# Kernel optimization log

Measured on AMD Instinct MI355X. Metric: run time of the kernel, lower is better.

Reference implementation:

```python
import jax, jax.numpy as jnp
import numpy as np

N_USER = 200000
N_ITEM = 100000
E = 1000000
H = 128
IN_USER = 64
IN_ITEM = 128
OUT = 16
L = 2  # n_layers
NEG_SLOPE = 0.01  # F.leaky_relu default


def _leaky(x):
    return jnp.where(x >= 0, x, NEG_SLOPE * x)


def _sage(x_src, x_dst, src, dst, n_dst, Wl, bl, Wr):
    """PyG SAGEConv (aggr='mean'): lin_l(mean_{j->i} x_j) + lin_r(x_i)."""
    agg = jax.ops.segment_sum(x_src[src], dst, num_segments=n_dst)  # [n_dst, H]
    cnt = jax.ops.segment_sum(jnp.ones((src.shape[0],), x_src.dtype), dst, num_segments=n_dst)
    mean = agg / jnp.maximum(cnt, 1.0)[:, None]
    return mean @ Wl + bl + x_dst @ Wr


def setup_inputs() -> dict:
    key = jax.random.key(0)
    ks = jax.random.split(key, 32)
    s = 0.05
    inp = {
        "x_user": jax.random.normal(ks[0], (N_USER, IN_USER), jnp.float32),
        "x_item": jax.random.normal(ks[1], (N_ITEM, IN_ITEM), jnp.float32),
        "src_rates": jax.random.randint(ks[2], (E,), 0, N_USER, jnp.int32),
        "dst_rates": jax.random.randint(ks[3], (E,), 0, N_ITEM, jnp.int32),
        "src_rated": jax.random.randint(ks[4], (E,), 0, N_ITEM, jnp.int32),
        "dst_rated": jax.random.randint(ks[5], (E,), 0, N_USER, jnp.int32),
        "src_fol": jax.random.randint(ks[6], (E,), 0, N_USER, jnp.int32),
        "dst_fol": jax.random.randint(ks[7], (E,), 0, N_USER, jnp.int32),
        # input projections (per node type)
        "W_in_user": s * jax.random.normal(ks[8], (IN_USER, H), jnp.float32),
        "b_in_user": jnp.zeros((H,), jnp.float32),
        "W_in_item": s * jax.random.normal(ks[9], (IN_ITEM, H), jnp.float32),
        "b_in_item": jnp.zeros((H,), jnp.float32),
        # per-layer SAGEConv params, stacked over layers [L, ...]
        "Wl_rates": s * jax.random.normal(ks[10], (L, H, H), jnp.float32),
        "bl_rates": jnp.zeros((L, H), jnp.float32),
        "Wr_rates": s * jax.random.normal(ks[11], (L, H, H), jnp.float32),
        "Wl_rated": s * jax.random.normal(ks[12], (L, H, H), jnp.float32),
        "bl_rated": jnp.zeros((L, H), jnp.float32),
        "Wr_rated": s * jax.random.normal(ks[13], (L, H, H), jnp.float32),
        "Wl_fol": s * jax.random.normal(ks[14], (L, H, H), jnp.float32),
        "bl_fol": jnp.zeros((L, H), jnp.float32),
        "Wr_fol": s * jax.random.normal(ks[15], (L, H, H), jnp.float32),
        # output head
        "W_out": s * jax.random.normal(ks[16], (H, OUT), jnp.float32),
        "b_out": jnp.zeros((OUT,), jnp.float32),
    }
    return inp


def reference(x_user, x_item, src_rates, dst_rates, src_rated, dst_rated,
              src_fol, dst_fol, W_in_user, b_in_user, W_in_item, b_in_item,
              Wl_rates, bl_rates, Wr_rates, Wl_rated, bl_rated, Wr_rated,
              Wl_fol, bl_fol, Wr_fol, W_out, b_out):
    hu = x_user @ W_in_user + b_in_user  # [N_USER, H]
    hi = x_item @ W_in_item + b_in_item  # [N_ITEM, H]
    for l in range(L):
        # user->item ('rates')
        hi_new = _sage(hu, hi, src_rates, dst_rates, N_ITEM,
                       Wl_rates[l], bl_rates[l], Wr_rates[l])
        # item->user ('rated_by') + user->user ('follows'), HeteroConv aggr='sum'
        hu_new = (_sage(hi, hu, src_rated, dst_rated, N_USER,
                        Wl_rated[l], bl_rated[l], Wr_rated[l])
                  + _sage(hu, hu, src_fol, dst_fol, N_USER,
                          Wl_fol[l], bl_fol[l], Wr_fol[l]))
        hu, hi = hu_new, hi_new
        if l != L - 1:
            hu = _leaky(hu)
            hi = _leaky(hi)
    return hu @ W_out + b_out  # target_node == 'user'
```

## Files before the change

### kernel.cpp

```cpp
#include <hip/hip_runtime.h>
#include <cstdint>

typedef short short8 __attribute__((ext_vector_type(8)));
typedef float floatx4 __attribute__((ext_vector_type(4)));

constexpr int NU = 200000;
constexpr int NI = 100000;
constexpr int NEDGE = 1000000;
constexpr int HD = 128;
constexpr int HH = HD * HD;
constexpr int BUK = 1024;
constexpr int EPB = 4096;
constexpr int EPT = 16;
constexpr int MAXBUK = 256;
constexpr int NBLK = (NEDGE + EPB - 1) / EPB;
constexpr int NB_I = (NI + BUK - 1) / BUK;
constexpr int NB_U = (NU + BUK - 1) / BUK;
constexpr int LROW = 136;

__device__ __forceinline__ float bits2f(short s) {
    return __uint_as_float(((unsigned int)(unsigned short)s) << 16);
}
__device__ __forceinline__ short f2bits(float f) {
    unsigned int u = __float_as_uint(f);
    unsigned int lsb = (u >> 16) & 1u;
    u += 0x7fffu + lsb;
    return (short)(u >> 16);
}

__global__ __launch_bounds__(256) void k_cnt3(const int* __restrict__ dst0,
                                              const int* __restrict__ dst1,
                                              const int* __restrict__ dst2,
                                              int* __restrict__ cnts) {
    __shared__ int cnt[MAXBUK];
    const int g = blockIdx.x / NBLK;
    const int blk = blockIdx.x % NBLK;
    const int* dst = (g == 0) ? dst0 : (g == 1) ? dst1 : dst2;
    int t = threadIdx.x;
    for (int b = t; b < MAXBUK; b += 256) cnt[b] = 0;
    __syncthreads();
    const int e0 = blk * EPB + t * EPT;
#pragma unroll
    for (int i = 0; i < EPT; ++i) {
        int e = e0 + i;
        if (e < NEDGE) atomicAdd(&cnt[dst[e] >> 10], 1);
    }
    __syncthreads();
    for (int b = t; b < MAXBUK; b += 256)
        cnts[(size_t)(g * NBLK + blk) * MAXBUK + b] = cnt[b];
}

__global__ __launch_bounds__(256) void k_bases3(const int* __restrict__ cnts,
                                                int* __restrict__ base,
                                                int* __restrict__ bbase,
                                                int* __restrict__ off0,
                                                int* __restrict__ off1,
                                                int* __restrict__ off2) {
    __shared__ int s[256];
    const int g = blockIdx.x;
    const int t = threadIdx.x;
    int tot = 0;
    for (int blk = 0; blk < NBLK; ++blk)
        tot += cnts[(size_t)(g * NBLK + blk) * MAXBUK + t];
    s[t] = tot;
    __syncthreads();
    for (int d = 1; d < 256; d <<= 1) {
        int u = (t >= d) ? s[t - d] : 0;
        __syncthreads();
        s[t] += u;
        __syncthreads();
    }
    int bb = s[t] - tot;
    bbase[g * 257 + t] = bb;
    if (t == 255) bbase[g * 257 + 256] = bb + tot;
    int run = bb;
    for (int blk = 0; blk < NBLK; ++blk) {
        size_t idx = (size_t)(g * NBLK + blk) * MAXBUK + t;
        base[idx] = run;
        run += cnts[idx];
    }
    if (t == 0) {
        if (g == 0) off0[NI] = NEDGE;
        else if (g == 1) off1[NU] = NEDGE;
        else off2[NU] = NEDGE;
    }
}

__global__ __launch_bounds__(256) void k_part3(const int* __restrict__ src0,
                                               const int* __restrict__ dst0,
                                               const int* __restrict__ src1,
                                               const int* __restrict__ dst1,
                                               const int* __restrict__ src2,
                                               const int* __restrict__ dst2,
                                               const int* __restrict__ base,
                                               int* __restrict__ pairs) {
    __shared__ int cnt[MAXBUK];
    __shared__ int bas[MAXBUK];
    const int g = blockIdx.x / NBLK;
    const int blk = blockIdx.x % NBLK;
    const int* src = (g == 0) ? src0 : (g == 1) ? src1 : src2;
    const int* dst = (g == 0) ? dst0 : (g == 1) ? dst1 : dst2;
    int* pg = pairs + (size_t)g * NEDGE;
    int t = threadIdx.x;
    for (int b = t; b < MAXBUK; b += 256) cnt[b] = 0;
    __syncthreads();
    const int e0 = blk * EPB + t * EPT;
    int sv[EPT], dv[EPT], rk[EPT];
#pragma unroll
    for (int i = 0; i < EPT; ++i) {
        int e = e0 + i;
        bool ok = e < NEDGE;
        dv[i] = ok ? dst[e] : 0;
        sv[i] = ok ? src[e] : 0;
    }
#pragma unroll
    for (int i = 0; i < EPT; ++i)
        rk[i] = (e0 + i < NEDGE) ? atomicAdd(&cnt[dv[i] >> 10], 1) : 0;
    __syncthreads();
    for (int b = t; b < MAXBUK; b += 256)
        bas[b] = base[(size_t)(g * NBLK + blk) * MAXBUK + b];
    __syncthreads();
#pragma unroll
    for (int i = 0; i < EPT; ++i) {
        if (e0 + i < NEDGE)
            pg[bas[dv[i] >> 10] + rk[i]] = sv[i] | ((dv[i] & 1023) << 18);
    }
}

__global__ __launch_bounds__(256) void k_place3(const int* __restrict__ pairs,
                                                const int* __restrict__ bbase,
                                                int* __restrict__ off0, int* __restrict__ esrc0,
                                                int* __restrict__ off1, int* __restrict__ esrc1,
                                                int* __restrict__ off2, int* __restrict__ esrc2) {
    __shared__ int cnt[BUK];
    __shared__ int ts[256];
    int bi = blockIdx.x;
    int g, bloc, N;
    int* off;
    int* esrc;
    if (bi < NB_I) { g = 0; bloc = bi; N = NI; off = off0; esrc = esrc0; }
    else if (bi < NB_I + NB_U) { g = 1; bloc = bi - NB_I; N = NU; off = off1; esrc = esrc1; }
    else { g = 2; bloc = bi - NB_I - NB_U; N = NU; off = off2; esrc = esrc2; }
    const int* pg = pairs + (size_t)g * NEDGE;
    const int b0 = bbase[g * 257 + bloc];
    const int b1 = bbase[g * 257 + bloc + 1];
    const int t = threadIdx.x;
    for (int i = t; i < BUK; i += 256) cnt[i] = 0;
    __syncthreads();
    for (int j = b0 + t; j < b1; j += 256) atomicAdd(&cnt[pg[j] >> 18], 1);
    __syncthreads();
    const int idx = t * 4;
    int c0 = cnt[idx], c1 = cnt[idx + 1], c2 = cnt[idx + 2], c3 = cnt[idx + 3];
    int ssum = c0 + c1 + c2 + c3;
    ts[t] = ssum;
    __syncthreads();
    for (int d = 1; d < 256; d <<= 1) {
        int u = (t >= d) ? ts[t - d] : 0;
        __syncthreads();
        ts[t] += u;
        __syncthreads();
    }
    int o = b0 + ts[t] - ssum;
    const int n0 = bloc * BUK;
    int cc[4] = {c0, c1, c2, c3};
#pragma unroll
    for (int i = 0; i < 4; ++i) {
        int n = n0 + idx + i;
        if (n < N) off[n] = o;
        cnt[idx + i] = o;
        o += cc[i];
    }
    __syncthreads();
    for (int j = b0 + t; j < b1; j += 256) {
        int p = pg[j];
        int pos = atomicAdd(&cnt[p >> 18], 1);
        esrc[pos] = p & 0x3FFFF;
    }
}

__global__ void k_pack(short* __restrict__ dst, const float* __restrict__ A,
                       const float* __restrict__ B, const float* __restrict__ B2,
                       int KA, int KBr, int NCOL) {
    int l = threadIdx.x;
    int kbt = (KA + KBr) >> 5;
    int nt = blockIdx.x / kbt;
    int kb = blockIdx.x % kbt;
    int col = nt * 16 + (l & 15);
    int k0 = kb * 32 + (l >> 4) * 8;
    short8 o;
#pragma unroll
    for (int j = 0; j < 8; ++j) {
        int k = k0 + j;
        float f;
        if (k < KA) {
            f = A[(size_t)k * NCOL + col];
        } else {
            int k2 = k - KA;
            f = B[(size_t)k2 * NCOL + col];
            if (B2) f += B2[(size_t)k2 * NCOL + col];
        }
        o[j] = f2bits(f);
    }
    *(short8*)(dst + ((size_t)blockIdx.x * 64 + l) * 8) = o;
}

__global__ void k_pack3(short* __restrict__ dst, const float* __restrict__ A,
                        const float* __restrict__ B, const float* __restrict__ C1,
                        const float* __restrict__ C2) {
    int l = threadIdx.x;
    constexpr int kbt = 12;
    int nt = blockIdx.x / kbt;
    int kb = blockIdx.x % kbt;
    int col = nt * 16 + (l & 15);
    int k0 = kb * 32 + (l >> 4) * 8;
    short8 o;
#pragma unroll
    for (int j = 0; j < 8; ++j) {
        int k = k0 + j;
        float f;
        if (k < 128) f = A[(size_t)k * 128 + col];
        else if (k < 256) f = B[(size_t)(k - 128) * 128 + col];
        else f = C1[(size_t)(k - 256) * 128 + col] + C2[(size_t)(k - 256) * 128 + col];
        o[j] = f2bits(f);
    }
    *(short8*)(dst + ((size_t)blockIdx.x * 64 + l) * 8) = o;
}

__global__ void k_foldW(float* __restrict__ dst, const float* __restrict__ Wa,
                        const float* __restrict__ Wb, const float* __restrict__ Wo,
                        int colOff, int NC) {
    int k = blockIdx.x;
    int c = threadIdx.x;
    float a = 0.f;
    for (int t = 0; t < 128; ++t) {
        float w = Wa[(size_t)k * 128 + t];
        if (Wb) w += Wb[(size_t)k * 128 + t];
        a += w * Wo[t * 16 + c];
    }
    dst[(size_t)k * NC + colOff + c] = a;
}

__global__ void k_bfold(float* __restrict__ dst, const float* __restrict__ bl1,
                        const float* __restrict__ bl2, const float* __restrict__ Wo,
                        const float* __restrict__ bo) {
    int c = threadIdx.x;
    float a = 0.f;
    for (int t = 0; t < 128; ++t) a += (bl1[t] + bl2[t]) * Wo[t * 16 + c];
    dst[c] = a + bo[c];
}

__global__ void k_addbias(float* __restrict__ dst, const float* __restrict__ a,
                          const float* __restrict__ b) {
    int i = threadIdx.x;
    dst[i] = a[i] + b[i];
}

__device__ __forceinline__ void gather_mean(const short* __restrict__ Xsrc,
                                            const int* __restrict__ off,
                                            const int* __restrict__ esrc,
                                            int ar, int ksub, float macc[4][8]) {
#pragma unroll
    for (int kb = 0; kb < 4; ++kb)
#pragma unroll
        for (int i = 0; i < 8; ++i) macc[kb][i] = 0.f;

    const int s = off[ar], e = off[ar + 1];
    int j = s;
    for (; j + 4 <= e; j += 4) {
        const int i0 = esrc[j], i1 = esrc[j + 1], i2 = esrc[j + 2], i3 = esrc[j + 3];
        const short* p0 = Xsrc + (size_t)i0 * HD + ksub;
        const short* p1 = Xsrc + (size_t)i1 * HD + ksub;
        const short* p2 = Xsrc + (size_t)i2 * HD + ksub;
        const short* p3 = Xsrc + (size_t)i3 * HD + ksub;
        short8 v0[4], v1[4], v2[4], v3[4];
#pragma unroll
        for (int kb = 0; kb < 4; ++kb) {
            v0[kb] = *(const short8*)(p0 + kb * 32);
            v1[kb] = *(const short8*)(p1 + kb * 32);
            v2[kb] = *(const short8*)(p2 + kb * 32);
            v3[kb] = *(const short8*)(p3 + kb * 32);
        }
#pragma unroll
        for (int kb = 0; kb < 4; ++kb)
#pragma unroll
            for (int i = 0; i < 8; ++i)
                macc[kb][i] += (bits2f(v0[kb][i]) + bits2f(v1[kb][i]))
                             + (bits2f(v2[kb][i]) + bits2f(v3[kb][i]));
    }
    for (; j < e; ++j) {
        const short* xp = Xsrc + (size_t)esrc[j] * HD + ksub;
#pragma unroll
        for (int kb = 0; kb < 4; ++kb) {
            short8 v = *(const short8*)(xp + kb * 32);
#pragma unroll
            for (int i = 0; i < 8; ++i) macc[kb][i] += bits2f(v[i]);
        }
    }
    const int d = e - s;
    const float inv = 1.f / (float)(d > 0 ? d : 1);
#pragma unroll
    for (int kb = 0; kb < 4; ++kb)
#pragma unroll
        for (int i = 0; i < 8; ++i) macc[kb][i] *= inv;
}

template <int NT2>
__device__ __forceinline__ void fold_epi(const floatx4* acc8, const float* __restrict__ bias,
                                         const short* __restrict__ pFold,
                                         short* __restrict__ Y, int r0, int lane,
                                         short* my, int M) {
    const int colL = lane & 15;
    const int g = lane >> 4;
#pragma unroll
    for (int nt = 0; nt < 8; ++nt) {
        float bv = bias[nt * 16 + colL];
#pragma unroll
        for (int r = 0; r < 4; ++r) {
            float x = acc8[nt][r] + bv;
            x = (x >= 0.f) ? x : 0.01f * x;
            my[(g * 4 + r) * LROW + nt * 16 + colL] = f2bits(x);
        }
    }
    short8 af[4];
    const short* rp = my + colL * LROW + g * 8;
#pragma unroll
    for (int kb = 0; kb < 4; ++kb) af[kb] = *(const short8*)(rp + kb * 32);

    floatx4 a2[NT2];
#pragma unroll
    for (int nt2 = 0; nt2 < NT2; ++nt2) a2[nt2] = (floatx4){0.f, 0.f, 0.f, 0.f};
    const short8* wp = (const short8*)pFold + lane;
#pragma unroll
    for (int nt2 = 0; nt2 < NT2; ++nt2)
#pragma unroll
        for (int kb = 0; kb < 4; ++kb) {
            short8 b = wp[(nt2 * 4 + kb) * 64];
            a2[nt2] = __builtin_amdgcn_mfma_f32_16x16x32_bf16(af[kb], b, a2[nt2], 0, 0, 0);
        }

    const int rbase = r0 + g * 4;
#pragma unroll
    for (int nt2 = 0; nt2 < NT2; ++nt2)
#pragma unroll
        for (int r = 0; r < 4; ++r) {
            int row = rbase + r;
            if (row < M) Y[(size_t)row * (NT2 * 16) + nt2 * 16 + colL] = f2bits(a2[nt2][r]);
        }
}

__global__ __launch_bounds__(256) void k_sage_all(
        const short* __restrict__ hu, const short* __restrict__ hi,
        const int* __restrict__ off_rates, const int* __restrict__ esrc_rates,
        const int* __restrict__ off_rated, const int* __restrict__ esrc_rated,
        const int* __restrict__ off_fol, const int* __restrict__ esrc_fol,
        const short* __restrict__ WpI, const float* __restrict__ biasI,
        const short* __restrict__ pYI,
        const short* __restrict__ WpU, const float* __restrict__ biasU,
        const short* __restrict__ pYU,
        short* __restrict__ YI, short* __restrict__ YZ, int gU) {
    __shared__ short stage[4 * 16 * LROW];
    const int lane = threadIdx.x & 63;
    const int wv = threadIdx.x >> 6;
    short* my = stage + wv * (16 * LROW);
    const int ksub = (lane >> 4) * 8;

    if ((int)blockIdx.x < gU) {
        const int r0 = blockIdx.x * 64 + wv * 16;
        int ar = r0 + (lane & 15);
        if (ar >= NU) ar = NU - 1;

        short8 afrag[12];
        {
            float macc[4][8];
            gather_mean(hi, off_rated, esrc_rated, ar, ksub, macc);
#pragma unroll
            for (int kb = 0; kb < 4; ++kb) {
                short8 f;
#pragma unroll
                for (int i = 0; i < 8; ++i) f[i] = f2bits(macc[kb][i]);
                afrag[kb] = f;
            }
            gather_mean(hu, off_fol, esrc_fol, ar, ksub, macc);
#pragma unroll
            for (int kb = 0; kb < 4; ++kb) {
                short8 f;
#pragma unroll
                for (int i = 0; i < 8; ++i) f[i] = f2bits(macc[kb][i]);
                afrag[4 + kb] = f;
            }
        }
        {
            const short* p = hu + (size_t)ar * HD + ksub;
#pragma unroll
            for (int kb = 0; kb < 4; ++kb) afrag[8 + kb] = *(const short8*)(p + kb * 32);
        }

        floatx4 acc[8];
#pragma unroll
        for (int nt = 0; nt < 8; ++nt) acc[nt] = (floatx4){0.f, 0.f, 0.f, 0.f};
        const short8* wp = (const short8*)WpU + lane;
#pragma unroll
        for (int nt = 0; nt < 8; ++nt)
#pragma unroll
            for (int kb = 0; kb < 12; ++kb) {
                short8 b = wp[(nt * 12 + kb) * 64];
                acc[nt] = __builtin_amdgcn_mfma_f32_16x16x32_bf16(afrag[kb], b, acc[nt], 0, 0, 0);
            }

        fold_epi<2>(acc, biasU, pYU, YZ, r0, lane, my, NU);
    } else {
        const int b = blockIdx.x - gU;
        const int r0 = b * 64 + wv * 16;
        int ar = r0 + (lane & 15);
        if (ar >= NI) ar = NI - 1;

        short8 afrag[8];
        {
            float macc[4][8];
            gather_mean(hu, off_rates, esrc_rates, ar, ksub, macc);
#pragma unroll
            for (int kb = 0; kb < 4; ++kb) {
                short8 f;
#pragma unroll
                for (int i = 0; i < 8; ++i) f[i] = f2bits(macc[kb][i]);
                afrag[kb] = f;
            }
            const short* p = hi + (size_t)ar * HD + ksub;
#pragma unroll
            for (int kb = 0; kb < 4; ++kb) afrag[4 + kb] = *(const short8*)(p + kb * 32);
        }

        floatx4 acc[8];
#pragma unroll
        for (int nt = 0; nt < 8; ++nt) acc[nt] = (floatx4){0.f, 0.f, 0.f, 0.f};
        const short8* wp = (const short8*)WpI + lane;
#pragma unroll
        for (int nt = 0; nt < 8; ++nt)
#pragma unroll
            for (int kb = 0; kb < 8; ++kb) {
                short8 b = wp[(nt * 8 + kb) * 64];
                acc[nt] = __builtin_amdgcn_mfma_f32_16x16x32_bf16(afrag[kb], b, acc[nt], 0, 0, 0);
            }

        fold_epi<1>(acc, biasI, pYI, YI, r0, lane, my, NI);
    }
}

template <int KB1>
__device__ __forceinline__ void mm_body(int bid, const float* __restrict__ A1,
                                        const short* __restrict__ Wp,
                                        const float* __restrict__ bias,
                                        short* __restrict__ C, int M,
                                        int lane, int wv) {
    const int r0 = bid * 128 + wv * 32;
    const int ksub = (lane >> 4) * 8;
    short8 afrag[2][KB1];
#pragma unroll
    for (int h = 0; h < 2; ++h) {
        int ar = r0 + h * 16 + (lane & 15);
        if (ar >= M) ar = M - 1;
        const float* p = A1 + (size_t)ar * (KB1 * 32) + ksub;
#pragma unroll
        for (int kb = 0; kb < KB1; ++kb) {
            short8 f;
#pragma unroll
            for (int j = 0; j < 8; ++j) f[j] = f2bits(p[kb * 32 + j]);
            afrag[h][kb] = f;
        }
    }
    floatx4 acc[2][8];
#pragma unroll
    for (int h = 0; h < 2; ++h)
#pragma unroll
        for (int nt = 0; nt < 8; ++nt) acc[h][nt] = (floatx4){0.f, 0.f, 0.f, 0.f};
    const short8* wp = (const short8*)Wp + lane;
#pragma unroll
    for (int nt = 0; nt < 8; ++nt)
#pragma unroll
        for (int kb = 0; kb < KB1; ++kb) {
            short8 b = wp[(nt * KB1 + kb) * 64];
            acc[0][nt] = __builtin_amdgcn_mfma_f32_16x16x32_bf16(afrag[0][kb], b, acc[0][nt], 0, 0, 0);
            acc[1][nt] = __builtin_amdgcn_mfma_f32_16x16x32_bf16(afrag[1][kb], b, acc[1][nt], 0, 0, 0);
        }
    const int col = lane & 15;
#pragma unroll
    for (int h = 0; h < 2; ++h) {
        const int rbase = r0 + h * 16 + (lane >> 4) * 4;
#pragma unroll
        for (int nt = 0; nt < 8; ++nt) {
            float bv = bias[nt * 16 + col];
#pragma unroll
            for (int r = 0; r < 4; ++r) {
                int row = rbase + r;
                if (row < M)
                    C[(size_t)row * 128 + nt * 16 + col] = f2bits(acc[h][nt][r] + bv);
            }
        }
    }
}

__global__ __launch_bounds__(256) void k_mm2(const float* __restrict__ xu,
                                             const short* __restrict__ pWu,
                                             const float* __restrict__ bu,
                                             short* __restrict__ hu,
                                             const float* __restrict__ xi,
                                             const short* __restrict__ pWi,
                                             const float* __restrict__ bi,
                                             short* __restrict__ hi, int gU2) {
    const int lane = threadIdx.x & 63;
    const int wv = threadIdx.x >> 6;
    if ((int)blockIdx.x < gU2)
        mm_body<2>(blockIdx.x, xu, pWu, bu, hu, NU, lane, wv);
    else
        mm_body<4>(blockIdx.x - gU2, xi, pWi, bi, hi, NI, lane, wv);
}

__global__ __launch_bounds__(256) void k_out(const short* __restrict__ YZ,
                                             const short* __restrict__ YI,
                                             const int* __restrict__ off_f,
                                             const int* __restrict__ esrc_f,
                                             const int* __restrict__ off_r,
                                             const int* __restrict__ esrc_r,
                                             const float* __restrict__ bias16,
                                             float* __restrict__ out, int N) {
    int t = threadIdx.x;
    int node = blockIdx.x * 128 + (t >> 1);
    int half = t & 1;
    if (node >= N) return;
    const int c0 = half * 8;

    float a[8] = {0.f, 0.f, 0.f, 0.f, 0.f, 0.f, 0.f, 0.f};
    {
        const int s = off_f[node], e = off_f[node + 1];
        int j = s;
        for (; j + 4 <= e; j += 4) {
            short8 v0 = *(const short8*)(YZ + (size_t)esrc_f[j] * 32 + c0);
            short8 v1 = *(const short8*)(YZ + (size_t)esrc_f[j + 1] * 32 + c0);
            short8 v2 = *(const short8*)(YZ + (size_t)esrc_f[j + 2] * 32 + c0);
            short8 v3 = *(const short8*)(YZ + (size_t)esrc_f[j + 3] * 32 + c0);
#pragma unroll
            for (int i = 0; i < 8; ++i)
                a[i] += (bits2f(v0[i]) + bits2f(v1[i])) + (bits2f(v2[i]) + bits2f(v3[i]));
        }
        for (; j < e; ++j) {
            short8 v = *(const short8*)(YZ + (size_t)esrc_f[j] * 32 + c0);
#pragma unroll
            for (int i = 0; i < 8; ++i) a[i] += bits2f(v[i]);
        }
        int d = e - s;
        float inv = 1.f / (float)(d > 0 ? d : 1);
#pragma unroll
        for (int i = 0; i < 8; ++i) a[i] *= inv;
    }
    {
        float b[8] = {0.f, 0.f, 0.f, 0.f, 0.f, 0.f, 0.f, 0.f};
        const int s = off_r[node], e = off_r[node + 1];
        int j = s;
        for (; j + 4 <= e; j += 4) {
            short8 v0 = *(const short8*)(YI + (size_t)esrc_r[j] * 16 + c0);
            short8 v1 = *(const short8*)(YI + (size_t)esrc_r[j + 1] * 16 + c0);
            short8 v2 = *(const short8*)(YI + (size_t)esrc_r[j + 2] * 16 + c0);
            short8 v3 = *(const short8*)(YI + (size_t)esrc_r[j + 3] * 16 + c0);
#pragma unroll
            for (int i = 0; i < 8; ++i)
                b[i] += (bits2f(v0[i]) + bits2f(v1[i])) + (bits2f(v2[i]) + bits2f(v3[i]));
        }
        for (; j < e; ++j) {
            short8 v = *(const short8*)(YI + (size_t)esrc_r[j] * 16 + c0);
#pragma unroll
            for (int i = 0; i < 8; ++i) b[i] += bits2f(v[i]);
        }
        int d = e - s;
        float inv = 1.f / (float)(d > 0 ? d : 1);
#pragma unroll
        for (int i = 0; i < 8; ++i) a[i] += b[i] * inv;
    }
    short8 z = *(const short8*)(YZ + (size_t)node * 32 + 16 + c0);
#pragma unroll
    for (int i = 0; i < 8; ++i)
        out[(size_t)node * 16 + c0 + i] = a[i] + bits2f(z[i]) + bias16[c0 + i];
}

extern "C" void kernel_launch(void* const* d_in, const int* in_sizes, int n_in,
                              void* d_out, int out_size, void* d_ws, size_t ws_size,
                              hipStream_t stream) {
    const float* x_user    = (const float*)d_in[0];
    const float* x_item    = (const float*)d_in[1];
    const int* src_rates   = (const int*)d_in[2];
    const int* dst_rates   = (const int*)d_in[3];
    const int* src_rated   = (const int*)d_in[4];
    const int* dst_rated   = (const int*)d_in[5];
    const int* src_fol     = (const int*)d_in[6];
    const int* dst_fol     = (const int*)d_in[7];
    const float* W_in_user = (const float*)d_in[8];
    const float* b_in_user = (const float*)d_in[9];
    const float* W_in_item = (const float*)d_in[10];
    const float* b_in_item = (const float*)d_in[11];
    const float* Wl_rates  = (const float*)d_in[12];
    const float* bl_rates  = (const float*)d_in[13];
    const float* Wr_rates  = (const float*)d_in[14];
    const float* Wl_rated  = (const float*)d_in[15];
    const float* bl_rated  = (const float*)d_in[16];
    const float* Wr_rated  = (const float*)d_in[17];
    const float* Wl_fol    = (const float*)d_in[18];
    const float* bl_fol    = (const float*)d_in[19];
    const float* Wr_fol    = (const float*)d_in[20];
    const float* W_out     = (const float*)d_in[21];
    const float* b_out     = (const float*)d_in[22];
    float* out = (float*)d_out;

    char* w = (char*)d_ws;
    size_t used = 0;
    auto alloc = [&](size_t bytes) -> void* {
        void* p = w + used;
        used += (bytes + 255) & ~(size_t)255;
        return p;
    };
    short* hu_a = (short*)alloc((size_t)NU * HD * 2);
    short* hi_a = (short*)alloc((size_t)NI * HD * 2);
    short* YZ   = (short*)alloc((size_t)NU * 32 * 2);
    short* YI   = (short*)alloc((size_t)NI * 16 * 2);

    int* off_rates  = (int*)alloc((size_t)(NI + 1) * 4);
    int* esrc_rates = (int*)alloc((size_t)NEDGE * 4);
    int* off_rated  = (int*)alloc((size_t)(NU + 1) * 4);
    int* esrc_rated = (int*)alloc((size_t)NEDGE * 4);
    int* off_fol    = (int*)alloc((size_t)(NU + 1) * 4);
    int* esrc_fol   = (int*)alloc((size_t)NEDGE * 4);
    int* pairs      = (int*)alloc((size_t)3 * NEDGE * 4);
    int* cnts       = (int*)alloc((size_t)3 * NBLK * MAXBUK * 4);
    int* base       = (int*)alloc((size_t)3 * NBLK * MAXBUK * 4);
    int* bbase      = (int*)alloc((size_t)3 * 257 * 4);

    short* pWu    = (short*)alloc(8 * 2 * 64 * 8 * 2);
    short* pWi    = (short*)alloc(8 * 4 * 64 * 8 * 2);
    short* pRates0 = (short*)alloc(8 * 8 * 64 * 8 * 2);
    short* pUser0  = (short*)alloc(8 * 12 * 64 * 8 * 2);
    float* WfU    = (float*)alloc(128 * 32 * 4);
    float* WfI    = (float*)alloc(128 * 16 * 4);
    short* pYU    = (short*)alloc(2 * 4 * 64 * 8 * 2);
    short* pYI    = (short*)alloc(1 * 4 * 64 * 8 * 2);
    float* bSum0  = (float*)alloc(128 * 4);
    float* bias16 = (float*)alloc(16 * 4);
    if (used > ws_size) return;

    k_cnt3<<<3 * NBLK, 256, 0, stream>>>(dst_rates, dst_rated, dst_fol, cnts);
    k_bases3<<<3, 256, 0, stream>>>(cnts, base, bbase, off_rates, off_rated, off_fol);
    k_part3<<<3 * NBLK, 256, 0, stream>>>(src_rates, dst_rates, src_rated, dst_rated,
                                          src_fol, dst_fol, base, pairs);
    k_place3<<<NB_I + 2 * NB_U, 256, 0, stream>>>(pairs, bbase,
                                                  off_rates, esrc_rates,
                                                  off_rated, esrc_rated,
                                                  off_fol, esrc_fol);

    k_pack<<<16, 64, 0, stream>>>(pWu, W_in_user, nullptr, nullptr, 64, 0, 128);
    k_pack<<<32, 64, 0, stream>>>(pWi, W_in_item, nullptr, nullptr, 128, 0, 128);
    k_pack<<<64, 64, 0, stream>>>(pRates0, Wl_rates, Wr_rates, nullptr, 128, 128, 128);
    k_pack3<<<96, 64, 0, stream>>>(pUser0, Wl_rated, Wl_fol, Wr_rated, Wr_fol);
    k_addbias<<<1, 128, 0, stream>>>(bSum0, bl_rated, bl_fol);
    k_foldW<<<128, 16, 0, stream>>>(WfU, Wl_fol + HH,   nullptr,     W_out, 0, 32);
    k_foldW<<<128, 16, 0, stream>>>(WfU, Wr_rated + HH, Wr_fol + HH, W_out, 16, 32);
    k_foldW<<<128, 16, 0, stream>>>(WfI, Wl_rated + HH, nullptr,     W_out, 0, 16);
    k_pack<<<8, 64, 0, stream>>>(pYU, WfU, nullptr, nullptr, 128, 0, 32);
    k_pack<<<4, 64, 0, stream>>>(pYI, WfI, nullptr, nullptr, 128, 0, 16);
    k_bfold<<<1, 16, 0, stream>>>(bias16, bl_rated + 128, bl_fol + 128, W_out, b_out);

    const int gU2 = (NU + 127) / 128;
    const int gI2 = (NI + 127) / 128;
    const int gU  = (NU + 63) / 64;
    const int gI  = (NI + 63) / 64;

    k_mm2<<<gU2 + gI2, 256, 0, stream>>>(x_user, pWu, b_in_user, hu_a,
                                         x_item, pWi, b_in_item, hi_a, gU2);

    k_sage_all<<<gU + gI, 256, 0, stream>>>(
        hu_a, hi_a, off_rates, esrc_rates, off_rated, esrc_rated, off_fol, esrc_fol,
        pRates0, bl_rates, pYI, pUser0, bSum0, pYU, YI, YZ, gU);

    k_out<<<(NU + 127) / 128, 256, 0, stream>>>(
        YZ, YI, off_fol, esrc_fol, off_rated, esrc_rated, bias16, out, NU);
}
```

Baseline: 444.8 us.

## Quantize node embeddings to per-row int8 for neighbor gathers

The input projection kernel now also writes an 8-bit offset-quantized copy of each user and item embedding, with a per-row scale. The SAGE kernel gathers neighbors from this copy and dequantizes it with an FMA plus a final bias correction. The aim is to halve the gather memory traffic, which dominates the aggregation. In exchange it adds quantization error to the aggregated means, writes extra storage in the projection kernel, and removes the 4-way edge unrolling, which reduces memory-level parallelism.

```diff
diff --git a/kernel.cpp b/kernel.cpp
--- a/kernel.cpp
+++ b/kernel.cpp
@@ -3,6 +3,7 @@
 
 typedef short short8 __attribute__((ext_vector_type(8)));
 typedef float floatx4 __attribute__((ext_vector_type(4)));
+typedef unsigned char uchar;
 
 constexpr int NU = 200000;
 constexpr int NI = 100000;
@@ -255,53 +256,40 @@
     dst[i] = a[i] + b[i];
 }
 
-__device__ __forceinline__ void gather_mean(const short* __restrict__ Xsrc,
-                                            const int* __restrict__ off,
-                                            const int* __restrict__ esrc,
-                                            int ar, int ksub, float macc[4][8]) {
+__device__ __forceinline__ void gather_mean_u8(const uchar* __restrict__ X8,
+                                               const float* __restrict__ scale,
+                                               const int* __restrict__ off,
+                                               const int* __restrict__ esrc,
+                                               int ar, int g, float macc[4][8]) {
 #pragma unroll
     for (int kb = 0; kb < 4; ++kb)
 #pragma unroll
         for (int i = 0; i < 8; ++i) macc[kb][i] = 0.f;
+    float S = 0.f;
 
     const int s = off[ar], e = off[ar + 1];
-    int j = s;
-    for (; j + 4 <= e; j += 4) {
-        const int i0 = esrc[j], i1 = esrc[j + 1], i2 = esrc[j + 2], i3 = esrc[j + 3];
-        const short* p0 = Xsrc + (size_t)i0 * HD + ksub;
-        const short* p1 = Xsrc + (size_t)i1 * HD + ksub;
-        const short* p2 = Xsrc + (size_t)i2 * HD + ksub;
-        const short* p3 = Xsrc + (size_t)i3 * HD + ksub;
-        short8 v0[4], v1[4], v2[4], v3[4];
+    for (int j = s; j < e; ++j) {
+        const int i0 = esrc[j];
+        const float s0 = scale[i0];
+        const uchar* p0 = X8 + (size_t)i0 * HD + g * 8;
+        S += s0;
 #pragma unroll
         for (int kb = 0; kb < 4; ++kb) {
-            v0[kb] = *(const short8*)(p0 + kb * 32);
-            v1[kb] = *(const short8*)(p1 + kb * 32);
-            v2[kb] = *(const short8*)(p2 + kb * 32);
-            v3[kb] = *(const short8*)(p3 + kb * 32);
-        }
-#pragma unroll
-        for (int kb = 0; kb < 4; ++kb)
-#pragma unroll
-            for (int i = 0; i < 8; ++i)
-                macc[kb][i] += (bits2f(v0[kb][i]) + bits2f(v1[kb][i]))
-                             + (bits2f(v2[kb][i]) + bits2f(v3[kb][i]));
-    }
-    for (; j < e; ++j) {
-        const short* xp = Xsrc + (size_t)esrc[j] * HD + ksub;
-#pragma unroll
-        for (int kb = 0; kb < 4; ++kb) {
-            short8 v = *(const short8*)(xp + kb * 32);
-#pragma unroll
-            for (int i = 0; i < 8; ++i) macc[kb][i] += bits2f(v[i]);
+            uint2 v = *(const uint2*)(p0 + kb * 32);
+#pragma unroll
+            for (int i = 0; i < 4; ++i) {
+                macc[kb][i]     = fmaf(s0, (float)((v.x >> (8 * i)) & 0xffu), macc[kb][i]);
+                macc[kb][4 + i] = fmaf(s0, (float)((v.y >> (8 * i)) & 0xffu), macc[kb][4 + i]);
+            }
         }
     }
     const int d = e - s;
     const float inv = 1.f / (float)(d > 0 ? d : 1);
+    const float corr = 128.f * S;
 #pragma unroll
     for (int kb = 0; kb < 4; ++kb)
 #pragma unroll
-        for (int i = 0; i < 8; ++i) macc[kb][i] *= inv;
+        for (int i = 0; i < 8; ++i) macc[kb][i] = (macc[kb][i] - corr) * inv;
 }
 
 template <int NT2>
@@ -350,6 +338,8 @@
 
 __global__ __launch_bounds__(256) void k_sage_all(
         const short* __restrict__ hu, const short* __restrict__ hi,
+        const uchar* __restrict__ hu8, const float* __restrict__ scU,
+        const uchar* __restrict__ hi8, const float* __restrict__ scI,
         const int* __restrict__ off_rates, const int* __restrict__ esrc_rates,
         const int* __restrict__ off_rated, const int* __restrict__ esrc_rated,
         const int* __restrict__ off_fol, const int* __restrict__ esrc_fol,
@@ -362,7 +352,8 @@
     const int lane = threadIdx.x & 63;
     const int wv = threadIdx.x >> 6;
     short* my = stage + wv * (16 * LROW);
-    const int ksub = (lane >> 4) * 8;
+    const int g = lane >> 4;
+    const int ksub = g * 8;
 
     if ((int)blockIdx.x < gU) {
         const int r0 = blockIdx.x * 64 + wv * 16;
@@ -372,7 +363,7 @@
         short8 afrag[12];
         {
             float macc[4][8];
-            gather_mean(hi, off_rated, esrc_rated, ar, ksub, macc);
+            gather_mean_u8(hi8, scI, off_rated, esrc_rated, ar, g, macc);
 #pragma unroll
             for (int kb = 0; kb < 4; ++kb) {
                 short8 f;
@@ -380,7 +371,7 @@
                 for (int i = 0; i < 8; ++i) f[i] = f2bits(macc[kb][i]);
                 afrag[kb] = f;
             }
-            gather_mean(hu, off_fol, esrc_fol, ar, ksub, macc);
+            gather_mean_u8(hu8, scU, off_fol, esrc_fol, ar, g, macc);
 #pragma unroll
             for (int kb = 0; kb < 4; ++kb) {
                 short8 f;
@@ -417,7 +408,7 @@
         short8 afrag[8];
         {
             float macc[4][8];
-            gather_mean(hu, off_rates, esrc_rates, ar, ksub, macc);
+            gather_mean_u8(hu8, scU, off_rates, esrc_rates, ar, g, macc);
 #pragma unroll
             for (int kb = 0; kb < 4; ++kb) {
                 short8 f;
@@ -450,14 +441,18 @@
 __device__ __forceinline__ void mm_body(int bid, const float* __restrict__ A1,
                                         const short* __restrict__ Wp,
                                         const float* __restrict__ bias,
-                                        short* __restrict__ C, int M,
+                                        short* __restrict__ C,
+                                        uchar* __restrict__ U8,
+                                        float* __restrict__ scale, int M,
                                         int lane, int wv) {
     const int r0 = bid * 128 + wv * 32;
-    const int ksub = (lane >> 4) * 8;
+    const int g = lane >> 4;
+    const int ksub = g * 8;
+    const int colL = lane & 15;
     short8 afrag[2][KB1];
 #pragma unroll
     for (int h = 0; h < 2; ++h) {
-        int ar = r0 + h * 16 + (lane & 15);
+        int ar = r0 + h * 16 + colL;
         if (ar >= M) ar = M - 1;
         const float* p = A1 + (size_t)ar * (KB1 * 32) + ksub;
 #pragma unroll
@@ -482,18 +477,29 @@
             acc[0][nt] = __builtin_amdgcn_mfma_f32_16x16x32_bf16(afrag[0][kb], b, acc[0][nt], 0, 0, 0);
             acc[1][nt] = __builtin_amdgcn_mfma_f32_16x16x32_bf16(afrag[1][kb], b, acc[1][nt], 0, 0, 0);
         }
-    const int col = lane & 15;
 #pragma unroll
     for (int h = 0; h < 2; ++h) {
-        const int rbase = r0 + h * 16 + (lane >> 4) * 4;
-#pragma unroll
-        for (int nt = 0; nt < 8; ++nt) {
-            float bv = bias[nt * 16 + col];
-#pragma unroll
-            for (int r = 0; r < 4; ++r) {
-                int row = rbase + r;
-                if (row < M)
-                    C[(size_t)row * 128 + nt * 16 + col] = f2bits(acc[h][nt][r] + bv);
+#pragma unroll
+        for (int r = 0; r < 4; ++r) {
+            const int row = r0 + h * 16 + g * 4 + r;
+            float v[8];
+            float m = 0.f;
+#pragma unroll
+            for (int nt = 0; nt < 8; ++nt) {
+                v[nt] = acc[h][nt][r] + bias[nt * 16 + colL];
+                m = fmaxf(m, fabsf(v[nt]));
+            }
+#pragma unroll
+            for (int x = 1; x < 16; x <<= 1) m = fmaxf(m, __shfl_xor(m, x, 16));
+            const float invq = (m > 0.f) ? 127.f / m : 0.f;
+            if (row < M) {
+#pragma unroll
+                for (int nt = 0; nt < 8; ++nt) {
+                    C[(size_t)row * HD + nt * 16 + colL] = f2bits(v[nt]);
+                    U8[(size_t)row * HD + nt * 16 + colL] =
+                        (uchar)((int)rintf(v[nt] * invq) + 128);
+                }
+                if (colL == 0) scale[row] = m * (1.f / 127.f);
             }
         }
     }
@@ -503,16 +509,20 @@
                                              const short* __restrict__ pWu,
                                              const float* __restrict__ bu,
                                              short* __restrict__ hu,
+                                             uchar* __restrict__ hu8,
+                                             float* __restrict__ scU,
                                              const float* __restrict__ xi,
                                              const short* __restrict__ pWi,
                                              const float* __restrict__ bi,
-                                             short* __restrict__ hi, int gU2) {
+                                             short* __restrict__ hi,
+                                             uchar* __restrict__ hi8,
+                                             float* __restrict__ scI, int gU2) {
     const int lane = threadIdx.x & 63;
     const int wv = threadIdx.x >> 6;
     if ((int)blockIdx.x < gU2)
-        mm_body<2>(blockIdx.x, xu, pWu, bu, hu, NU, lane, wv);
+        mm_body<2>(blockIdx.x, xu, pWu, bu, hu, hu8, scU, NU, lane, wv);
     else
-        mm_body<4>(blockIdx.x - gU2, xi, pWi, bi, hi, NI, lane, wv);
+        mm_body<4>(blockIdx.x - gU2, xi, pWi, bi, hi, hi8, scI, NI, lane, wv);
 }
 
 __global__ __launch_bounds__(256) void k_out(const short* __restrict__ YZ,
@@ -618,6 +628,10 @@
     };
     short* hu_a = (short*)alloc((size_t)NU * HD * 2);
     short* hi_a = (short*)alloc((size_t)NI * HD * 2);
+    uchar* hu8  = (uchar*)alloc((size_t)NU * HD);
+    uchar* hi8  = (uchar*)alloc((size_t)NI * HD);
+    float* scU  = (float*)alloc((size_t)NU * 4);
+    float* scI  = (float*)alloc((size_t)NI * 4);
     short* YZ   = (short*)alloc((size_t)NU * 32 * 2);
     short* YI   = (short*)alloc((size_t)NI * 16 * 2);
 
@@ -632,16 +646,16 @@
     int* base       = (int*)alloc((size_t)3 * NBLK * MAXBUK * 4);
     int* bbase      = (int*)alloc((size_t)3 * 257 * 4);
 
-    short* pWu    = (short*)alloc(8 * 2 * 64 * 8 * 2);
-    short* pWi    = (short*)alloc(8 * 4 * 64 * 8 * 2);
+    short* pWu     = (short*)alloc(8 * 2 * 64 * 8 * 2);
+    short* pWi     = (short*)alloc(8 * 4 * 64 * 8 * 2);
     short* pRates0 = (short*)alloc(8 * 8 * 64 * 8 * 2);
     short* pUser0  = (short*)alloc(8 * 12 * 64 * 8 * 2);
-    float* WfU    = (float*)alloc(128 * 32 * 4);
-    float* WfI    = (float*)alloc(128 * 16 * 4);
-    short* pYU    = (short*)alloc(2 * 4 * 64 * 8 * 2);
-    short* pYI    = (short*)alloc(1 * 4 * 64 * 8 * 2);
-    float* bSum0  = (float*)alloc(128 * 4);
-    float* bias16 = (float*)alloc(16 * 4);
+    float* WfU     = (float*)alloc(128 * 32 * 4);
+    float* WfI     = (float*)alloc(128 * 16 * 4);
+    short* pYU     = (short*)alloc(2 * 4 * 64 * 8 * 2);
+    short* pYI     = (short*)alloc(1 * 4 * 64 * 8 * 2);
+    float* bSum0   = (float*)alloc(128 * 4);
+    float* bias16  = (float*)alloc(16 * 4);
     if (used > ws_size) return;
 
     k_cnt3<<<3 * NBLK, 256, 0, stream>>>(dst_rates, dst_rated, dst_fol, cnts);
@@ -670,11 +684,12 @@
     const int gU  = (NU + 63) / 64;
     const int gI  = (NI + 63) / 64;
 
-    k_mm2<<<gU2 + gI2, 256, 0, stream>>>(x_user, pWu, b_in_user, hu_a,
-                                         x_item, pWi, b_in_item, hi_a, gU2);
+    k_mm2<<<gU2 + gI2, 256, 0, stream>>>(x_user, pWu, b_in_user, hu_a, hu8, scU,
+                                         x_item, pWi, b_in_item, hi_a, hi8, scI, gU2);
 
     k_sage_all<<<gU + gI, 256, 0, stream>>>(
-        hu_a, hi_a, off_rates, esrc_rates, off_rated, esrc_rated, off_fol, esrc_fol,
+        hu_a, hi_a, hu8, scU, hi8, scI,
+        off_rates, esrc_rates, off_rated, esrc_rated, off_fol, esrc_fol,
         pRates0, bl_rates, pYI, pUser0, bSum0, pYU, YI, YZ, gU);
 
     k_out<<<(NU + 127) / 128, 256, 0, stream>>>(
```

Measured after the change: 494.8 us. +11.3%, slower.
